# Performance work log

Hardware: AMD Instinct MI355X
Metric: run time of the kernel (lower is better)

## Reference

```python
import jax, jax.numpy as jnp
import numpy as np


def _attention(q, k, v, causal):
    # q,k,v: (B, S, H, D) -> matches flash_attn_func input layout
    B, Sq, H, D = q.shape
    Sk = k.shape[1]
    scale = 1.0 / jnp.sqrt(jnp.asarray(D, dtype=q.dtype))
    # scores: (B, H, Sq, Sk)
    scores = jnp.einsum('bqhd,bkhd->bhqk', q, k) * scale
    if causal:
        # position i attends to j <= i (standard causal mask, Sq == Sk here)
        mask = jnp.tril(jnp.ones((Sq, Sk), dtype=bool))
        scores = jnp.where(mask[None, None], scores, jnp.asarray(-jnp.inf, dtype=scores.dtype))
    probs = jax.nn.softmax(scores, axis=-1)
    out = jnp.einsum('bhqk,bkhd->bqhd', probs, v)
    return out


def setup_inputs() -> dict:
    key = jax.random.key(0)
    kq, kk, kv = jax.random.split(key, 3)
    B, S, H, D = 2, 2048, 16, 128
    q = jax.random.normal(kq, (B, S, H, D), dtype=jnp.float32)
    k = jax.random.normal(kk, (B, S, H, D), dtype=jnp.float32)
    v = jax.random.normal(kv, (B, S, H, D), dtype=jnp.float32)
    return {"q": q, "k": k, "v": v, "causal": 1}


def reference(q, k, v, causal):
    return _attention(q, k, v, bool(causal))
```

## Files before the change

kernel.cpp:

```cpp
#include <hip/hip_runtime.h>

typedef short bf16x8 __attribute__((ext_vector_type(8)));
typedef float f32x16 __attribute__((ext_vector_type(16)));

constexpr int S = 2048;
constexpr int H = 16;
constexpr int D = 128;
constexpr int BM = 128;
constexpr int BN = 64;
constexpr int KSTR = 136;
constexpr int PSTRW = 36;
constexpr int TILE = 8192;


__device__ inline unsigned int pk2(float a, float b) {
    unsigned int ua = __builtin_bit_cast(unsigned int, a);
    unsigned int ub = __builtin_bit_cast(unsigned int, b);
    ua += 0x7fffu + ((ua >> 16) & 1u);
    ub += 0x7fffu + ((ub >> 16) & 1u);
    return (ua >> 16) | (ub & 0xffff0000u);
}

__device__ __forceinline__ void gld16(const unsigned short* g, unsigned short* l) {
    __builtin_amdgcn_global_load_lds(
        (const __attribute__((address_space(1))) unsigned int*)g,
        (__attribute__((address_space(3))) unsigned int*)l, 16, 0, 0);
}

__global__ __launch_bounds__(256) void cvt_k(const float* __restrict__ src,
                                             unsigned short* __restrict__ dst) {
    const int tid = threadIdx.x;
    const int t   = blockIdx.x;
    const int bh  = blockIdx.y;
    const int b = bh >> 4, h = bh & 15;
    unsigned short* out = dst + ((size_t)bh * 32 + t) * TILE;
    const size_t rb = ((size_t)(b * S + t * 64) * H + h) * D;
    #pragma unroll
    for (int u = 0; u < 4; ++u) {
        const int dlin = u * 256 + tid;
        const int g = dlin >> 6;
        const int s = dlin & 63;
        const int r = s >> 4;
        const int csrc = (s & 15) ^ (2 * r);
        const float* p = src + rb + (size_t)(g * 4 + r) * (H * D) + csrc * 8;
        float4 f0 = *(const float4*)p;
        float4 f1 = *(const float4*)(p + 4);
        unsigned int w[4];
        w[0] = pk2(f0.x, f0.y); w[1] = pk2(f0.z, f0.w);
        w[2] = pk2(f1.x, f1.y); w[3] = pk2(f1.z, f1.w);
        *(uint4*)(out + dlin * 8) = *(const uint4*)w;
    }
}

__global__ __launch_bounds__(256) void cvt_vt(const float* __restrict__ V,
                                              unsigned short* __restrict__ dst) {
    __shared__ unsigned short Vl[64 * KSTR];
    const int tid = threadIdx.x;
    const int j  = blockIdx.x;
    const int bh = blockIdx.y;
    const int b = bh >> 4, h = bh & 15;
    #pragma unroll
    for (int u = 0; u < 4; ++u) {
        const int c   = tid + 256 * u;
        const int n   = c >> 4;
        const int off = (c & 15) * 8;
        const float* p = V + ((size_t)(b * S + j * 64 + n) * H + h) * D + off;
        float4 f0 = *(const float4*)p;
        float4 f1 = *(const float4*)(p + 4);
        unsigned int w[4];
        w[0] = pk2(f0.x, f0.y); w[1] = pk2(f0.z, f0.w);
        w[2] = pk2(f1.x, f1.y); w[3] = pk2(f1.z, f1.w);
        *(uint4*)&Vl[n * KSTR + off] = *(const uint4*)w;
    }
    __syncthreads();
    const int d  = tid >> 1;
    const int kh = (tid & 1) * 32;
    unsigned short tmp[32];
    #pragma unroll
    for (int m = 0; m < 32; ++m) {
        const int kp = kh + m;
        const int n  = (kp >> 1) + (kp & 1) * 32;
        tmp[m] = Vl[n * KSTR + d];
    }
    unsigned short* out = dst + ((size_t)bh * 32 + j) * TILE;
    const int g = d >> 3, rho = d & 7;
    #pragma unroll
    for (int uu = 0; uu < 4; ++uu) {
        const int cc = (kh >> 3) + uu;
        *(uint4*)(out + g * 512 + (rho * 8 + (cc ^ rho)) * 8) = *(const uint4*)&tmp[uu * 8];
    }
}

__global__ __launch_bounds__(256, 2) void fa_fwd(
    const float* __restrict__ Q,
    const unsigned short* __restrict__ Kb,
    const unsigned short* __restrict__ Vtb,
    const int* __restrict__ causal_p,
    float* __restrict__ Op)
{
    __shared__ unsigned short Kl[2][TILE];
    __shared__ unsigned short Vt[TILE];
    __shared__ unsigned int   Pl[4 * 32 * PSTRW];

    const int tid  = threadIdx.x;
    const int wave = tid >> 6;
    const int lane = tid & 63;
    const int ln   = lane & 31;
    const int half = lane >> 5;

    int bh, qblk;
    if (gridDim.y == 32) {
        const int lid = blockIdx.x + (blockIdx.y << 4);
        const int xcd = lid & 7;
        const int ii  = lid >> 3;
        bh = (xcd << 2) + (ii & 3);
        const int qp = ii >> 2;
        qblk = (qp < 8) ? qp : 23 - qp;
    } else {
        bh = blockIdx.y;
        qblk = blockIdx.x;
    }
    const int b = bh >> 4;
    const int h = bh & 15;

    const int q0    = qblk * BM;
    const int qrow0 = q0 + wave * 32;
    const int causal = *causal_p;
    const float cfold = 0.12751743f;

    const unsigned short* Ksrc = Kb  + (size_t)bh * (32 * TILE);
    const unsigned short* Vsrc = Vtb + (size_t)bh * (32 * TILE);
    const int sg   = wave * 4;
    const int loff = lane * 8;

    #pragma unroll
    for (int qq = 0; qq < 4; ++qq)
        gld16(Ksrc + (sg + qq) * 512 + loff, &Kl[0][(sg + qq) * 512]);
    #pragma unroll
    for (int qq = 0; qq < 4; ++qq)
        gld16(Vsrc + (sg + qq) * 512 + loff, &Vt[(sg + qq) * 512]);

    bf16x8 qf[8];
    {
        const size_t rowoff = ((size_t)(b * S + qrow0 + ln) * H + h) * D;
        #pragma unroll
        for (int c = 0; c < 8; ++c) {
            float4 f0 = *(const float4*)(Q + rowoff + c * 16 + half * 8);
            float4 f1 = *(const float4*)(Q + rowoff + c * 16 + half * 8 + 4);
            unsigned int t[4];
            t[0] = pk2(f0.x * cfold, f0.y * cfold);
            t[1] = pk2(f0.z * cfold, f0.w * cfold);
            t[2] = pk2(f1.x * cfold, f1.y * cfold);
            t[3] = pk2(f1.z * cfold, f1.w * cfold);
            qf[c] = *(const bf16x8*)t;
        }
    }

    f32x16 o[4];
    #pragma unroll
    for (int dt = 0; dt < 4; ++dt)
        #pragma unroll
        for (int r = 0; r < 16; ++r) o[dt][r] = 0.0f;

    float l_st[16];
    #pragma unroll
    for (int r = 0; r < 16; ++r) l_st[r] = 0.0f;

    const int jmax = causal ? ((q0 + BM - 1) >> 6) : (S / BN - 1);
    unsigned int* Pw = &Pl[wave * 32 * PSTRW];

    const int kxr   = 2 * (ln & 3);
    const int kbase = (ln >> 2) * 512 + (ln & 3) * 128;
    const int vrho  = ln & 7;
    const int vbase = (ln >> 3) * 512;

    asm volatile("s_waitcnt vmcnt(0)" ::: "memory");

    int cur = 0;
    for (int j = 0; j <= jmax; ++j) {
        asm volatile("s_waitcnt vmcnt(4)" ::: "memory");
        __builtin_amdgcn_s_barrier();

        if (j < jmax) {
            const unsigned short* ks = Ksrc + (size_t)(j + 1) * TILE;
            #pragma unroll
            for (int qq = 0; qq < 4; ++qq)
                gld16(ks + (sg + qq) * 512 + loff, &Kl[cur ^ 1][(sg + qq) * 512]);
        }

        f32x16 sacc[2];
        __builtin_amdgcn_s_setprio(1);
        #pragma unroll
        for (int nt = 0; nt < 2; ++nt) {
            #pragma unroll
            for (int r = 0; r < 16; ++r) sacc[nt][r] = 0.0f;
            const unsigned short* kl = &Kl[cur][nt * 4096 + kbase];
            #pragma unroll
            for (int c = 0; c < 8; ++c) {
                uint4 raw = *(const uint4*)(kl + ((c * 2 + half) ^ kxr) * 8);
                bf16x8 kf = *(const bf16x8*)&raw;
                sacc[nt] = __builtin_amdgcn_mfma_f32_32x32x16_bf16(qf[c], kf, sacc[nt], 0, 0, 0);
            }
        }
        __builtin_amdgcn_s_setprio(0);

        const bool need_mask = (causal != 0) && (j * BN + BN - 1 > qrow0);
        const int nbase = j * BN + ln;
        #pragma unroll
        for (int r = 0; r < 16; ++r) {
            const int rl  = (r & 3) + 8 * (r >> 2) + 4 * half;
            const int row = qrow0 + rl;
            float e0 = __builtin_amdgcn_exp2f(sacc[0][r]);
            float e1 = __builtin_amdgcn_exp2f(sacc[1][r]);
            if (need_mask) {
                if (nbase > row)      e0 = 0.0f;
                if (nbase + 32 > row) e1 = 0.0f;
            }
            l_st[r] += e0 + e1;
            Pw[rl * PSTRW + ln] = pk2(e0, e1);
        }

        if (j < jmax) asm volatile("s_waitcnt vmcnt(4)" ::: "memory");
        else          asm volatile("s_waitcnt vmcnt(0)" ::: "memory");
        __builtin_amdgcn_s_barrier();

        __builtin_amdgcn_s_setprio(1);
        #pragma unroll
        for (int c = 0; c < 4; ++c) {
            uint4 rawp = *(const uint4*)&Pw[ln * PSTRW + c * 8 + half * 4];
            bf16x8 pf = *(const bf16x8*)&rawp;
            const int cc = c * 2 + half;
            #pragma unroll
            for (int dt = 0; dt < 4; ++dt) {
                uint4 rawv = *(const uint4*)(Vt + dt * 2048 + vbase + (vrho * 8 + (cc ^ vrho)) * 8);
                bf16x8 vf = *(const bf16x8*)&rawv;
                o[dt] = __builtin_amdgcn_mfma_f32_32x32x16_bf16(pf, vf, o[dt], 0, 0, 0);
            }
        }
        __builtin_amdgcn_s_setprio(0);

        if (j < jmax) {
            asm volatile("s_waitcnt lgkmcnt(0)" ::: "memory");
            __builtin_amdgcn_s_barrier();
            const unsigned short* vs = Vsrc + (size_t)(j + 1) * TILE;
            #pragma unroll
            for (int qq = 0; qq < 4; ++qq)
                gld16(vs + (sg + qq) * 512 + loff, &Vt[(sg + qq) * 512]);
        }
        cur ^= 1;
    }

    #pragma unroll
    for (int r = 0; r < 16; ++r) {
        const int rl = (r & 3) + 8 * (r >> 2) + 4 * half;
        float rs = l_st[r];
        #pragma unroll
        for (int off = 16; off >= 1; off >>= 1)
            rs += __shfl_xor(rs, off);
        const float inv = 1.0f / rs;
        const size_t rowoff = ((size_t)(b * S + qrow0 + rl) * H + h) * D;
        #pragma unroll
        for (int dt = 0; dt < 4; ++dt)
            Op[rowoff + dt * 32 + ln] = o[dt][r] * inv;
    }
}

extern "C" void kernel_launch(void* const* d_in, const int* in_sizes, int n_in,
                              void* d_out, int out_size, void* d_ws, size_t ws_size,
                              hipStream_t stream) {
    const int B = in_sizes[0] / (S * H * D);
    unsigned short* Kb  = (unsigned short*)d_ws;
    unsigned short* Vtb = Kb + (size_t)B * S * H * D;

    cvt_k <<<dim3(S / 64, B * H), 256, 0, stream>>>((const float*)d_in[1], Kb);
    cvt_vt<<<dim3(S / 64, B * H), 256, 0, stream>>>((const float*)d_in[2], Vtb);
    fa_fwd<<<dim3(S / BM, B * H), 256, 0, stream>>>(
        (const float*)d_in[0], Kb, Vtb, (const int*)d_in[3], (float*)d_out);
}
```

Measured before the change: 213.4 us.

## Transpose S=KQ^T to keep P in registers, merge K/V conversion, stage output

Computes S transposed (K as the A operand) so each lane owns a query column, which lets the probabilities be packed into bf16 MFMA operands directly from registers and removes the P round-trip through LDS and one barrier. K and V conversion kernels are merged into one launch, with K and V tile layouts reswizzled to match. K and V tiles are now both double-buffered and prefetched together, and each wave skips fully masked causal tiles. The row-sum reduction shrinks to a single cross-half shuffle, and output is staged through shared memory for coalesced float4 stores. Costs: a larger shared allocation, which may reduce occupancy, and a full vmcnt(0) wait every iteration.

```diff
diff --git a/kernel.cpp b/kernel.cpp
--- a/kernel.cpp
+++ b/kernel.cpp
@@ -7,10 +7,9 @@
 constexpr int H = 16;
 constexpr int D = 128;
 constexpr int BM = 128;
-constexpr int BN = 64;
+constexpr int TILE = 8192;
 constexpr int KSTR = 136;
-constexpr int PSTRW = 36;
-constexpr int TILE = 8192;
+constexpr int EPAD = 132;
 
 
 __device__ inline unsigned int pk2(float a, float b) {
@@ -27,44 +26,40 @@
         (__attribute__((address_space(3))) unsigned int*)l, 16, 0, 0);
 }
 
-__global__ __launch_bounds__(256) void cvt_k(const float* __restrict__ src,
-                                             unsigned short* __restrict__ dst) {
+__global__ __launch_bounds__(256) void cvt_kv(const float* __restrict__ K,
+                                              const float* __restrict__ V,
+                                              unsigned short* __restrict__ Kb,
+                                              unsigned short* __restrict__ Vtb) {
+    __shared__ unsigned short Vl[64 * KSTR];
     const int tid = threadIdx.x;
     const int t   = blockIdx.x;
     const int bh  = blockIdx.y;
     const int b = bh >> 4, h = bh & 15;
-    unsigned short* out = dst + ((size_t)bh * 32 + t) * TILE;
-    const size_t rb = ((size_t)(b * S + t * 64) * H + h) * D;
+    const size_t base = ((size_t)(b * S + t * 64) * H + h) * D;
+
+    unsigned short* outK = Kb + ((size_t)bh * 32 + t) * TILE;
     #pragma unroll
     for (int u = 0; u < 4; ++u) {
         const int dlin = u * 256 + tid;
-        const int g = dlin >> 6;
-        const int s = dlin & 63;
-        const int r = s >> 4;
-        const int csrc = (s & 15) ^ (2 * r);
-        const float* p = src + rb + (size_t)(g * 4 + r) * (H * D) + csrc * 8;
+        const int grp = dlin >> 7;
+        const int s   = dlin & 127;
+        const int rho = s >> 4;
+        const int c   = (s & 15) ^ rho;
+        const float* p = K + base + (size_t)(grp * 8 + rho) * (H * D) + c * 8;
         float4 f0 = *(const float4*)p;
         float4 f1 = *(const float4*)(p + 4);
         unsigned int w[4];
         w[0] = pk2(f0.x, f0.y); w[1] = pk2(f0.z, f0.w);
         w[2] = pk2(f1.x, f1.y); w[3] = pk2(f1.z, f1.w);
-        *(uint4*)(out + dlin * 8) = *(const uint4*)w;
-    }
-}
-
-__global__ __launch_bounds__(256) void cvt_vt(const float* __restrict__ V,
-                                              unsigned short* __restrict__ dst) {
-    __shared__ unsigned short Vl[64 * KSTR];
-    const int tid = threadIdx.x;
-    const int j  = blockIdx.x;
-    const int bh = blockIdx.y;
-    const int b = bh >> 4, h = bh & 15;
+        *(uint4*)(outK + dlin * 8) = *(const uint4*)w;
+    }
+
     #pragma unroll
     for (int u = 0; u < 4; ++u) {
-        const int c   = tid + 256 * u;
-        const int n   = c >> 4;
-        const int off = (c & 15) * 8;
-        const float* p = V + ((size_t)(b * S + j * 64 + n) * H + h) * D + off;
+        const int cidx = tid + 256 * u;
+        const int n    = cidx >> 4;
+        const int off  = (cidx & 15) * 8;
+        const float* p = V + base + (size_t)n * (H * D) + off;
         float4 f0 = *(const float4*)p;
         float4 f1 = *(const float4*)(p + 4);
         unsigned int w[4];
@@ -73,21 +68,22 @@
         *(uint4*)&Vl[n * KSTR + off] = *(const uint4*)w;
     }
     __syncthreads();
+
     const int d  = tid >> 1;
     const int kh = (tid & 1) * 32;
     unsigned short tmp[32];
     #pragma unroll
     for (int m = 0; m < 32; ++m) {
-        const int kp = kh + m;
-        const int n  = (kp >> 1) + (kp & 1) * 32;
-        tmp[m] = Vl[n * KSTR + d];
-    }
-    unsigned short* out = dst + ((size_t)bh * 32 + j) * TILE;
+        const int sig = kh + m;
+        const int k = (sig & ~12) | ((sig & 4) << 1) | ((sig & 8) >> 1);
+        tmp[m] = Vl[k * KSTR + d];
+    }
+    unsigned short* outV = Vtb + ((size_t)bh * 32 + t) * TILE;
     const int g = d >> 3, rho = d & 7;
     #pragma unroll
     for (int uu = 0; uu < 4; ++uu) {
         const int cc = (kh >> 3) + uu;
-        *(uint4*)(out + g * 512 + (rho * 8 + (cc ^ rho)) * 8) = *(const uint4*)&tmp[uu * 8];
+        *(uint4*)(outV + g * 512 + (rho * 8 + (cc ^ rho)) * 8) = *(const uint4*)&tmp[uu * 8];
     }
 }
 
@@ -98,9 +94,9 @@
     const int* __restrict__ causal_p,
     float* __restrict__ Op)
 {
-    __shared__ unsigned short Kl[2][TILE];
-    __shared__ unsigned short Vt[TILE];
-    __shared__ unsigned int   Pl[4 * 32 * PSTRW];
+    __shared__ __align__(16) unsigned char smem[4 * 32 * EPAD * 4];
+    unsigned short* KlB = (unsigned short*)smem;
+    unsigned short* VtB = (unsigned short*)smem + 2 * TILE;
 
     const int tid  = threadIdx.x;
     const int wave = tid >> 6;
@@ -135,10 +131,10 @@
 
     #pragma unroll
     for (int qq = 0; qq < 4; ++qq)
-        gld16(Ksrc + (sg + qq) * 512 + loff, &Kl[0][(sg + qq) * 512]);
+        gld16(Ksrc + (sg + qq) * 512 + loff, KlB + (sg + qq) * 512);
     #pragma unroll
     for (int qq = 0; qq < 4; ++qq)
-        gld16(Vsrc + (sg + qq) * 512 + loff, &Vt[(sg + qq) * 512]);
+        gld16(Vsrc + (sg + qq) * 512 + loff, VtB + (sg + qq) * 512);
 
     bf16x8 qf[8];
     {
@@ -161,108 +157,112 @@
     for (int dt = 0; dt < 4; ++dt)
         #pragma unroll
         for (int r = 0; r < 16; ++r) o[dt][r] = 0.0f;
-
-    float l_st[16];
-    #pragma unroll
-    for (int r = 0; r < 16; ++r) l_st[r] = 0.0f;
-
-    const int jmax = causal ? ((q0 + BM - 1) >> 6) : (S / BN - 1);
-    unsigned int* Pw = &Pl[wave * 32 * PSTRW];
-
-    const int kxr   = 2 * (ln & 3);
-    const int kbase = (ln >> 2) * 512 + (ln & 3) * 128;
-    const int vrho  = ln & 7;
-    const int vbase = (ln >> 3) * 512;
+    float l = 0.0f;
+
+    const int jmax = causal ? ((q0 + BM - 1) >> 6) : (S / 64 - 1);
+
+    const int kb   = (ln >> 3) * 1024 + (ln & 7) * 128;
+    const int krho = ln & 7;
+    const int vg   = (ln >> 3) * 512;
+    const int vrho = ln & 7;
 
     asm volatile("s_waitcnt vmcnt(0)" ::: "memory");
+    __builtin_amdgcn_s_barrier();
 
     int cur = 0;
     for (int j = 0; j <= jmax; ++j) {
-        asm volatile("s_waitcnt vmcnt(4)" ::: "memory");
-        __builtin_amdgcn_s_barrier();
-
         if (j < jmax) {
             const unsigned short* ks = Ksrc + (size_t)(j + 1) * TILE;
+            const unsigned short* vs = Vsrc + (size_t)(j + 1) * TILE;
+            unsigned short* kd = KlB + (cur ^ 1) * TILE;
+            unsigned short* vd = VtB + (cur ^ 1) * TILE;
             #pragma unroll
             for (int qq = 0; qq < 4; ++qq)
-                gld16(ks + (sg + qq) * 512 + loff, &Kl[cur ^ 1][(sg + qq) * 512]);
-        }
-
-        f32x16 sacc[2];
-        __builtin_amdgcn_s_setprio(1);
-        #pragma unroll
-        for (int nt = 0; nt < 2; ++nt) {
-            #pragma unroll
-            for (int r = 0; r < 16; ++r) sacc[nt][r] = 0.0f;
-            const unsigned short* kl = &Kl[cur][nt * 4096 + kbase];
-            #pragma unroll
-            for (int c = 0; c < 8; ++c) {
-                uint4 raw = *(const uint4*)(kl + ((c * 2 + half) ^ kxr) * 8);
-                bf16x8 kf = *(const bf16x8*)&raw;
-                sacc[nt] = __builtin_amdgcn_mfma_f32_32x32x16_bf16(qf[c], kf, sacc[nt], 0, 0, 0);
+                gld16(ks + (sg + qq) * 512 + loff, kd + (sg + qq) * 512);
+            #pragma unroll
+            for (int qq = 0; qq < 4; ++qq)
+                gld16(vs + (sg + qq) * 512 + loff, vd + (sg + qq) * 512);
+        }
+
+        const bool active = (!causal) || (j * 64 <= qrow0 + 31);
+        if (active) {
+            const unsigned short* Klc = KlB + cur * TILE;
+            const unsigned short* Vtc = VtB + cur * TILE;
+
+            f32x16 sacc[2];
+            __builtin_amdgcn_s_setprio(1);
+            #pragma unroll
+            for (int nt = 0; nt < 2; ++nt) {
+                #pragma unroll
+                for (int r = 0; r < 16; ++r) sacc[nt][r] = 0.0f;
+                const unsigned short* kl = Klc + nt * 4096 + kb;
+                #pragma unroll
+                for (int c = 0; c < 8; ++c) {
+                    uint4 raw = *(const uint4*)(kl + (((2 * c + half) ^ krho) << 3));
+                    bf16x8 kf = *(const bf16x8*)&raw;
+                    sacc[nt] = __builtin_amdgcn_mfma_f32_32x32x16_bf16(kf, qf[c], sacc[nt], 0, 0, 0);
+                }
             }
-        }
-        __builtin_amdgcn_s_setprio(0);
-
-        const bool need_mask = (causal != 0) && (j * BN + BN - 1 > qrow0);
-        const int nbase = j * BN + ln;
+            __builtin_amdgcn_s_setprio(0);
+
+            float p[32];
+            const int thr  = qrow0 + ln - j * 64;
+            const bool full = (!causal) || (j * 64 + 63 <= qrow0);
+            #pragma unroll
+            for (int nt = 0; nt < 2; ++nt)
+                #pragma unroll
+                for (int r = 0; r < 16; ++r) {
+                    float e = __builtin_amdgcn_exp2f(sacc[nt][r]);
+                    if (!full) {
+                        const int kl_ = nt * 32 + (r & 3) + 8 * (r >> 2) + 4 * half;
+                        if (kl_ > thr) e = 0.0f;
+                    }
+                    l += e;
+                    p[nt * 16 + r] = e;
+                }
+
+            __builtin_amdgcn_s_setprio(1);
+            #pragma unroll
+            for (int win = 0; win < 4; ++win) {
+                unsigned int pw[4];
+                #pragma unroll
+                for (int d2 = 0; d2 < 4; ++d2)
+                    pw[d2] = pk2(p[win * 8 + 2 * d2], p[win * 8 + 2 * d2 + 1]);
+                bf16x8 pf = *(const bf16x8*)pw;
+                const int voff = ((vrho * 8) + ((win * 2 + half) ^ vrho)) << 3;
+                #pragma unroll
+                for (int dt = 0; dt < 4; ++dt) {
+                    uint4 raw = *(const uint4*)(Vtc + dt * 2048 + vg + voff);
+                    bf16x8 vf = *(const bf16x8*)&raw;
+                    o[dt] = __builtin_amdgcn_mfma_f32_32x32x16_bf16(vf, pf, o[dt], 0, 0, 0);
+                }
+            }
+            __builtin_amdgcn_s_setprio(0);
+        }
+
+        asm volatile("s_waitcnt vmcnt(0)" ::: "memory");
+        __builtin_amdgcn_s_barrier();
+        cur ^= 1;
+    }
+
+    const float lt  = l + __shfl_xor(l, 32);
+    const float inv = 1.0f / lt;
+    float* sc = (float*)smem + wave * (32 * EPAD);
+    #pragma unroll
+    for (int dt = 0; dt < 4; ++dt)
         #pragma unroll
         for (int r = 0; r < 16; ++r) {
-            const int rl  = (r & 3) + 8 * (r >> 2) + 4 * half;
-            const int row = qrow0 + rl;
-            float e0 = __builtin_amdgcn_exp2f(sacc[0][r]);
-            float e1 = __builtin_amdgcn_exp2f(sacc[1][r]);
-            if (need_mask) {
-                if (nbase > row)      e0 = 0.0f;
-                if (nbase + 32 > row) e1 = 0.0f;
-            }
-            l_st[r] += e0 + e1;
-            Pw[rl * PSTRW + ln] = pk2(e0, e1);
-        }
-
-        if (j < jmax) asm volatile("s_waitcnt vmcnt(4)" ::: "memory");
-        else          asm volatile("s_waitcnt vmcnt(0)" ::: "memory");
-        __builtin_amdgcn_s_barrier();
-
-        __builtin_amdgcn_s_setprio(1);
-        #pragma unroll
-        for (int c = 0; c < 4; ++c) {
-            uint4 rawp = *(const uint4*)&Pw[ln * PSTRW + c * 8 + half * 4];
-            bf16x8 pf = *(const bf16x8*)&rawp;
-            const int cc = c * 2 + half;
-            #pragma unroll
-            for (int dt = 0; dt < 4; ++dt) {
-                uint4 rawv = *(const uint4*)(Vt + dt * 2048 + vbase + (vrho * 8 + (cc ^ vrho)) * 8);
-                bf16x8 vf = *(const bf16x8*)&rawv;
-                o[dt] = __builtin_amdgcn_mfma_f32_32x32x16_bf16(pf, vf, o[dt], 0, 0, 0);
-            }
-        }
-        __builtin_amdgcn_s_setprio(0);
-
-        if (j < jmax) {
-            asm volatile("s_waitcnt lgkmcnt(0)" ::: "memory");
-            __builtin_amdgcn_s_barrier();
-            const unsigned short* vs = Vsrc + (size_t)(j + 1) * TILE;
-            #pragma unroll
-            for (int qq = 0; qq < 4; ++qq)
-                gld16(vs + (sg + qq) * 512 + loff, &Vt[(sg + qq) * 512]);
-        }
-        cur ^= 1;
-    }
-
-    #pragma unroll
-    for (int r = 0; r < 16; ++r) {
-        const int rl = (r & 3) + 8 * (r >> 2) + 4 * half;
-        float rs = l_st[r];
-        #pragma unroll
-        for (int off = 16; off >= 1; off >>= 1)
-            rs += __shfl_xor(rs, off);
-        const float inv = 1.0f / rs;
-        const size_t rowoff = ((size_t)(b * S + qrow0 + rl) * H + h) * D;
-        #pragma unroll
-        for (int dt = 0; dt < 4; ++dt)
-            Op[rowoff + dt * 32 + ln] = o[dt][r] * inv;
-    }
+            const int d = dt * 32 + (r & 3) + 8 * (r >> 2) + 4 * half;
+            sc[ln * EPAD + d] = o[dt][r] * inv;
+        }
+    __syncthreads();
+    const int row = tid >> 1;
+    const int dh  = (tid & 1) * 64;
+    const float* s2 = (float*)smem + (row >> 5) * (32 * EPAD) + (row & 31) * EPAD + dh;
+    float* op = Op + ((size_t)(b * S + q0 + row) * H + h) * D + dh;
+    #pragma unroll
+    for (int u = 0; u < 16; ++u)
+        *(float4*)(op + u * 4) = *(const float4*)(s2 + u * 4);
 }
 
 extern "C" void kernel_launch(void* const* d_in, const int* in_sizes, int n_in,
@@ -272,8 +272,8 @@
     unsigned short* Kb  = (unsigned short*)d_ws;
     unsigned short* Vtb = Kb + (size_t)B * S * H * D;
 
-    cvt_k <<<dim3(S / 64, B * H), 256, 0, stream>>>((const float*)d_in[1], Kb);
-    cvt_vt<<<dim3(S / 64, B * H), 256, 0, stream>>>((const float*)d_in[2], Vtb);
+    cvt_kv<<<dim3(S / 64, B * H), 256, 0, stream>>>(
+        (const float*)d_in[1], (const float*)d_in[2], Kb, Vtb);
     fa_fwd<<<dim3(S / BM, B * H), 256, 0, stream>>>(
         (const float*)d_in[0], Kb, Vtb, (const int*)d_in[3], (float*)d_out);
 }
```

After: 201.0 us. 1.06x faster.
